# Performance work log

Measured on AMD Instinct MI355X. Metric: run time of the kernel, lower is better.

Reference implementation:

```python
import jax, jax.numpy as jnp
import numpy as np

EPS = 1e-4
GROUPS = 8


def setup_inputs() -> dict:
    key = jax.random.key(0)
    k1, k2 = jax.random.split(key)
    N, C, H, W = 64, 512, 32, 32
    x = jax.random.normal(k1, (N, C, H, W), dtype=jnp.float32)
    weight = jax.random.uniform(k2, (C, 1), dtype=jnp.float32)  # torch reset: uniform_()
    bias = jnp.zeros((C, 1), dtype=jnp.float32)
    return {"x": x, "weight": weight, "bias": bias}


def _whiten_group(cov):
    # cov: [L, L] symmetric PSD. torch.svd on symmetric PSD gives descending
    # eigenvalues e and eigenvectors in v's columns.
    _, e, vh = jnp.linalg.svd(cov)
    v = vh.T
    L = e.shape[0]
    # Faithful reproduction of the source's counter_i logic:
    # counter_i = 1 unless some eigenvalue <= eps, then counter_i = first such j + 1.
    hit = e <= EPS
    counter = jnp.where(jnp.any(hit), jnp.argmax(hit) + 1, 1)
    keep = jnp.arange(L) < counter
    w = jnp.where(keep, jax.lax.rsqrt(e), 0.0)
    # subspace = sum_j v_j * rsqrt(e_j) * v_j^T over kept j
    return (v * w[None, :]) @ v.T


def reference(x, weight, bias):
    N, C, H, W = x.shape
    G = GROUPS
    L = C // G
    M = N * H * W
    xf = jnp.transpose(x, (1, 0, 2, 3)).reshape(C, M)  # [C, N*H*W]
    mu = xf.mean(1, keepdims=True)
    xc = xf - mu
    xg = xc.reshape(G, L, M)
    # Diagonal blocks of (x x^T / M + eps*I): [G, L, L]
    cov = jnp.einsum('glm,gkm->glk', xg, xg) / M + EPS * jnp.eye(L, dtype=xg.dtype)
    sub = jax.vmap(_whiten_group)(cov)  # [G, L, L]
    xr = jnp.einsum('glk,gkm->glm', sub, xg).reshape(C, M)
    xr = xr * weight + bias
    return jnp.transpose(xr.reshape(C, N, H, W), (1, 0, 2, 3))
```

## Files before the change

### kernel.cpp

```cpp
#include <hip/hip_runtime.h>

#define HW    1024
#define C_CH  512


__global__ __launch_bounds__(256, 8) void cov_kernel(const float* __restrict__ x,
                                                     float* __restrict__ Spart,
                                                     float* __restrict__ chansum) {
  const int ks = blockIdx.x & 3;
  const int n  = (blockIdx.x >> 2) & 63;
  const int g  = blockIdx.x >> 8;
  __shared__ __align__(16) float As[4096];
  const int t  = threadIdx.x;
  const int ti = t >> 4;
  const int tj = t & 15;
  float acc[4][4];
#pragma unroll
  for (int r = 0; r < 4; r++)
#pragma unroll
    for (int s = 0; s < 4; s++) acc[r][s] = 0.f;
  float rsum = 0.f;

  const float* base = x + ((size_t)(n * C_CH + g * 64)) * HW;
  const int rlo = t >> 4;
  const int cc  = t & 15;

  for (int chunk = 0; chunk < 4; chunk++) {
    const int k0 = ks * 256 + chunk * 64;
#pragma unroll
    for (int s = 0; s < 4; s++) {
      const int row = 16 * s + rlo;
      const float4 v = *(const float4*)(base + (size_t)row * HW + k0 + 4 * cc);
      const int w0 = 4 * ((row >> 2) ^ cc) + (row & 3);
      As[(4 * cc + 0) * 64 + w0] = v.x;
      As[(4 * cc + 1) * 64 + w0] = v.y;
      As[(4 * cc + 2) * 64 + w0] = v.z;
      As[(4 * cc + 3) * 64 + w0] = v.w;
    }
    __syncthreads();
#pragma unroll 16
    for (int kk = 0; kk < 64; kk++) {
      const int kq = kk >> 2;
      const float4 a = *(const float4*)&As[kk * 64 + 4 * (ti ^ kq)];
      const float4 b = *(const float4*)&As[kk * 64 + 4 * (tj ^ kq)];
      acc[0][0] += a.x * b.x; acc[0][1] += a.x * b.y; acc[0][2] += a.x * b.z; acc[0][3] += a.x * b.w;
      acc[1][0] += a.y * b.x; acc[1][1] += a.y * b.y; acc[1][2] += a.y * b.z; acc[1][3] += a.y * b.w;
      acc[2][0] += a.z * b.x; acc[2][1] += a.z * b.y; acc[2][2] += a.z * b.z; acc[2][3] += a.z * b.w;
      acc[3][0] += a.w * b.x; acc[3][1] += a.w * b.y; acc[3][2] += a.w * b.z; acc[3][3] += a.w * b.w;
    }
    if (t < 64) {
      float s2 = 0.f;
#pragma unroll 16
      for (int kk = 0; kk < 64; kk++)
        s2 += As[kk * 64 + 4 * ((t >> 2) ^ (kk >> 2)) + (t & 3)];
      rsum += s2;
    }
    __syncthreads();
  }

  float* P = Spart + ((size_t)(g * 256 + n * 4 + ks)) * 4096;
#pragma unroll
  for (int r = 0; r < 4; r++) {
    float4 w4;
    w4.x = acc[r][0]; w4.y = acc[r][1]; w4.z = acc[r][2]; w4.w = acc[r][3];
    *(float4*)&P[(4 * ti + r) * 64 + 4 * tj] = w4;
  }
  if (t < 64) atomicAdd(&chansum[g * 64 + t], rsum);
}

__global__ __launch_bounds__(256) void reduce_kernel(const float* __restrict__ Spart,
                                                     float* __restrict__ S) {
  const int q   = blockIdx.x >> 7;
  const int idx = (blockIdx.x & 127) * 256 + threadIdx.x;
  const int g   = idx >> 12;
  const int e   = idx & 4095;
  const float* P = Spart + ((size_t)(g * 256 + q * 64)) * 4096 + e;
  float s = 0.f;
#pragma unroll 8
  for (int p = 0; p < 64; p++) s += P[(size_t)p * 4096];
  atomicAdd(&S[idx], s);
}

__global__ __launch_bounds__(256) void eigen_kernel(
    const float* __restrict__ S, const float* __restrict__ chansum,
    const float* __restrict__ weight, const float* __restrict__ bias,
    float* __restrict__ v0f, float* __restrict__ w2, float* __restrict__ b2) {
  const int g = blockIdx.x;
  __shared__ __align__(16) float Bf[64 * 68];
  __shared__ double Cd[64][65];
  __shared__ double vv[64], uu[64];
  __shared__ double dred;
  __shared__ float f32red;
  __shared__ int ired;
  const int t  = threadIdx.x;
  const int ti = t >> 4, tj = t & 15;
  const double Minv = 1.0 / 65536.0;

  for (int idx = t; idx < 4096; idx += 256) {
    const int i = idx >> 6, j = idx & 63;
    const double mui = (double)chansum[g * 64 + i] * Minv;
    const double muj = (double)chansum[g * 64 + j] * Minv;
    Cd[i][j] = (double)S[g * 4096 + idx] * Minv - mui * muj + (i == j ? 1e-4 : 0.0);
  }
  __syncthreads();
  if (t < 64) {
    double d = Cd[t][t];
#pragma unroll
    for (int off = 32; off; off >>= 1) d = fmin(d, __shfl_down(d, off));
    if (t == 0) f32red = (float)(0.49 * fmax(d, 0.0));
  }
  __syncthreads();
  const float sg = f32red;
  for (int idx = t; idx < 4096; idx += 256) {
    const int i = idx >> 6, j = idx & 63;
    Bf[i * 68 + j] = (float)Cd[i][j] - (i == j ? sg : 0.f);
  }
  __syncthreads();

  for (int it = 0; it < 12; it++) {
    if (t < 64) {
      float tr = Bf[t * 68 + t];
#pragma unroll
      for (int off = 32; off; off >>= 1) tr += __shfl_down(tr, off);
      if (t == 0) f32red = 1.f / tr;
    }
    __syncthreads();
    const float sc = f32red, scl = sc * sc;
    float acc[4][4];
#pragma unroll
    for (int r = 0; r < 4; r++)
#pragma unroll
      for (int s = 0; s < 4; s++) acc[r][s] = 0.f;
#pragma unroll 16
    for (int kk = 0; kk < 64; kk++) {
      const float4 a = *(const float4*)&Bf[kk * 68 + 4 * ti];
      const float4 b = *(const float4*)&Bf[kk * 68 + 4 * tj];
      acc[0][0] += a.x * b.x; acc[0][1] += a.x * b.y; acc[0][2] += a.x * b.z; acc[0][3] += a.x * b.w;
      acc[1][0] += a.y * b.x; acc[1][1] += a.y * b.y; acc[1][2] += a.y * b.z; acc[1][3] += a.y * b.w;
      acc[2][0] += a.z * b.x; acc[2][1] += a.z * b.y; acc[2][2] += a.z * b.z; acc[2][3] += a.z * b.w;
      acc[3][0] += a.w * b.x; acc[3][1] += a.w * b.y; acc[3][2] += a.w * b.z; acc[3][3] += a.w * b.w;
    }
    __syncthreads();
#pragma unroll
    for (int r = 0; r < 4; r++) {
      float4 w4;
      w4.x = acc[r][0] * scl; w4.y = acc[r][1] * scl;
      w4.z = acc[r][2] * scl; w4.w = acc[r][3] * scl;
      *(float4*)&Bf[(4 * ti + r) * 68 + 4 * tj] = w4;
    }
    __syncthreads();
  }

  if (t < 64) {
    float d = Bf[t * 68 + t];
    int bj = t;
#pragma unroll
    for (int off = 32; off; off >>= 1) {
      const float od = __shfl_down(d, off);
      const int   oj = __shfl_down(bj, off);
      if (od > d) { d = od; bj = oj; }
    }
    if (t == 0) ired = bj;
  }
  __syncthreads();
  const int jstar = ired;
  if (t < 64) vv[t] = (double)Bf[t * 68 + jstar];
  __syncthreads();

  for (int pi = 0; pi < 3; pi++) {
    if (t < 64) {
      double s = 0.0;
      for (int k = 0; k < 64; k++) s += Cd[t][k] * vv[k];
      uu[t] = s;
    }
    __syncthreads();
    if (t < 64) {
      double q = uu[t] * uu[t];
#pragma unroll
      for (int off = 32; off; off >>= 1) q += __shfl_down(q, off);
      if (t == 0) dred = 1.0 / sqrt(q);
    }
    __syncthreads();
    if (t < 64) vv[t] = uu[t] * dred;
    __syncthreads();
  }
  if (t < 64) {
    double s = 0.0;
    for (int k = 0; k < 64; k++) s += Cd[t][k] * vv[k];
    uu[t] = s;
  }
  __syncthreads();
  if (t < 64) {
    double q = vv[t] * uu[t];
#pragma unroll
    for (int off = 32; off; off >>= 1) q += __shfl_down(q, off);
    if (t == 0) dred = 1.0 / sqrt(q);
  }
  __syncthreads();
  const double rsl = dred;
  double w2v = 0.0;
  if (t < 64) {
    const int c = g * 64 + t;
    v0f[c] = (float)vv[t];
    w2v = (double)weight[c] * rsl * vv[t];
    w2[c] = (float)w2v;
  }
  __syncthreads();
  if (t < 64) {
    double q = vv[t] * ((double)chansum[g * 64 + t] * Minv);
#pragma unroll
    for (int off = 32; off; off >>= 1) q += __shfl_down(q, off);
    if (t == 0) dred = q;
  }
  __syncthreads();
  if (t < 64) {
    const int c = g * 64 + t;
    b2[c] = (float)((double)bias[c] - w2v * dred);
  }
}

__global__ __launch_bounds__(256, 8) void apply_kernel(
    const float* __restrict__ x, const float* __restrict__ v0f,
    const float* __restrict__ w2, const float* __restrict__ b2,
    float* __restrict__ out) {
  const int q = blockIdx.x & 3;
  const int n = (blockIdx.x >> 2) & 63;
  const int g = blockIdx.x >> 8;
  __shared__ float vs[64], wsh[64], bsh[64];
  const int t = threadIdx.x;
  if (t < 64) {
    vs[t]  = v0f[g * 64 + t];
    wsh[t] = w2[g * 64 + t];
    bsh[t] = b2[g * 64 + t];
  }
  __syncthreads();
  const size_t boff = ((size_t)(n * C_CH + g * 64)) * HW + q * 256 + t;
  const float* base = x + boff;
  float p = 0.f;
#pragma unroll 8
  for (int l = 0; l < 64; l++) p += vs[l] * base[(size_t)l * HW];
  float* ob = out + boff;
#pragma unroll 8
  for (int l = 0; l < 64; l++) ob[(size_t)l * HW] = wsh[l] * p + bsh[l];
}

extern "C" void kernel_launch(void* const* d_in, const int* in_sizes, int n_in,
                              void* d_out, int out_size, void* d_ws, size_t ws_size,
                              hipStream_t stream) {
  const float* x      = (const float*)d_in[0];
  const float* weight = (const float*)d_in[1];
  const float* bias   = (const float*)d_in[2];
  float* out = (float*)d_out;
  float* ws  = (float*)d_ws;

  float* S       = ws;
  float* chansum = ws + 32768;
  float* v0f     = ws + 33280;
  float* w2      = ws + 33792;
  float* b2      = ws + 34304;
  float* Spart   = out;

  hipMemsetAsync(d_ws, 0, (32768 + 512) * sizeof(float), stream);

  cov_kernel<<<dim3(2048), dim3(256), 0, stream>>>(x, Spart, chansum);
  reduce_kernel<<<dim3(512), dim3(256), 0, stream>>>(Spart, S);
  eigen_kernel<<<dim3(8), dim3(256), 0, stream>>>(S, chansum, weight, bias,
                                                  v0f, w2, b2);
  apply_kernel<<<dim3(2048), dim3(256), 0, stream>>>(x, v0f, w2, b2, out);
}
```

Baseline: 324.8 us.

## Exploit Gram symmetry, halve K-splits, drop atomics, vectorize apply kernel

The covariance and eigen power-iteration GEMMs now compute only the upper-triangular 4x4 tiles (136 of 256 threads active) and mirror them into the lower half on store, which halves the FMA work. The cov kernel splits K in two instead of four. This halves the partial-sum buffer, so the reduce kernel sums 128 partials per element with a plain store and no atomics or memset of S. The apply kernel processes a whole image plane per block with float4 loads and stores. The cost is idle threads in the GEMM loops and lower block counts and parallelism in cov, reduce and apply.

```diff
diff --git a/kernel.cpp b/kernel.cpp
--- a/kernel.cpp
+++ b/kernel.cpp
@@ -4,16 +4,21 @@
 #define C_CH  512
 
 
-__global__ __launch_bounds__(256, 8) void cov_kernel(const float* __restrict__ x,
+__global__ __launch_bounds__(256, 4) void cov_kernel(const float* __restrict__ x,
                                                      float* __restrict__ Spart,
                                                      float* __restrict__ chansum) {
-  const int ks = blockIdx.x & 3;
-  const int n  = (blockIdx.x >> 2) & 63;
-  const int g  = blockIdx.x >> 8;
+  const int ks = blockIdx.x & 1;
+  const int n  = (blockIdx.x >> 1) & 63;
+  const int g  = blockIdx.x >> 7;
   __shared__ __align__(16) float As[4096];
-  const int t  = threadIdx.x;
-  const int ti = t >> 4;
-  const int tj = t & 15;
+  const int t = threadIdx.x;
+
+  int ti = 0, rem = t;
+  while (ti < 16 && rem >= 16 - ti) { rem -= 16 - ti; ++ti; }
+  const bool act = (t < 136);
+  const int tj = act ? ti + rem : 0;
+  if (!act) ti = 0;
+
   float acc[4][4];
 #pragma unroll
   for (int r = 0; r < 4; r++)
@@ -25,8 +30,8 @@
   const int rlo = t >> 4;
   const int cc  = t & 15;
 
-  for (int chunk = 0; chunk < 4; chunk++) {
-    const int k0 = ks * 256 + chunk * 64;
+  for (int chunk = 0; chunk < 8; chunk++) {
+    const int k0 = ks * 512 + chunk * 64;
 #pragma unroll
     for (int s = 0; s < 4; s++) {
       const int row = 16 * s + rlo;
@@ -38,15 +43,17 @@
       As[(4 * cc + 3) * 64 + w0] = v.w;
     }
     __syncthreads();
+    if (act) {
 #pragma unroll 16
-    for (int kk = 0; kk < 64; kk++) {
-      const int kq = kk >> 2;
-      const float4 a = *(const float4*)&As[kk * 64 + 4 * (ti ^ kq)];
-      const float4 b = *(const float4*)&As[kk * 64 + 4 * (tj ^ kq)];
-      acc[0][0] += a.x * b.x; acc[0][1] += a.x * b.y; acc[0][2] += a.x * b.z; acc[0][3] += a.x * b.w;
-      acc[1][0] += a.y * b.x; acc[1][1] += a.y * b.y; acc[1][2] += a.y * b.z; acc[1][3] += a.y * b.w;
-      acc[2][0] += a.z * b.x; acc[2][1] += a.z * b.y; acc[2][2] += a.z * b.z; acc[2][3] += a.z * b.w;
-      acc[3][0] += a.w * b.x; acc[3][1] += a.w * b.y; acc[3][2] += a.w * b.z; acc[3][3] += a.w * b.w;
+      for (int kk = 0; kk < 64; kk++) {
+        const int kq = kk >> 2;
+        const float4 a = *(const float4*)&As[kk * 64 + 4 * (ti ^ kq)];
+        const float4 b = *(const float4*)&As[kk * 64 + 4 * (tj ^ kq)];
+        acc[0][0] += a.x * b.x; acc[0][1] += a.x * b.y; acc[0][2] += a.x * b.z; acc[0][3] += a.x * b.w;
+        acc[1][0] += a.y * b.x; acc[1][1] += a.y * b.y; acc[1][2] += a.y * b.z; acc[1][3] += a.y * b.w;
+        acc[2][0] += a.z * b.x; acc[2][1] += a.z * b.y; acc[2][2] += a.z * b.z; acc[2][3] += a.z * b.w;
+        acc[3][0] += a.w * b.x; acc[3][1] += a.w * b.y; acc[3][2] += a.w * b.z; acc[3][3] += a.w * b.w;
+      }
     }
     if (t < 64) {
       float s2 = 0.f;
@@ -58,27 +65,36 @@
     __syncthreads();
   }
 
-  float* P = Spart + ((size_t)(g * 256 + n * 4 + ks)) * 4096;
-#pragma unroll
-  for (int r = 0; r < 4; r++) {
-    float4 w4;
-    w4.x = acc[r][0]; w4.y = acc[r][1]; w4.z = acc[r][2]; w4.w = acc[r][3];
-    *(float4*)&P[(4 * ti + r) * 64 + 4 * tj] = w4;
+  float* P = Spart + ((size_t)(g * 128 + n * 2 + ks)) * 4096;
+  if (act) {
+#pragma unroll
+    for (int r = 0; r < 4; r++) {
+      float4 w4;
+      w4.x = acc[r][0]; w4.y = acc[r][1]; w4.z = acc[r][2]; w4.w = acc[r][3];
+      *(float4*)&P[(4 * ti + r) * 64 + 4 * tj] = w4;
+    }
+    if (ti != tj) {
+#pragma unroll
+      for (int s = 0; s < 4; s++) {
+        float4 w4;
+        w4.x = acc[0][s]; w4.y = acc[1][s]; w4.z = acc[2][s]; w4.w = acc[3][s];
+        *(float4*)&P[(4 * tj + s) * 64 + 4 * ti] = w4;
+      }
+    }
   }
   if (t < 64) atomicAdd(&chansum[g * 64 + t], rsum);
 }
 
 __global__ __launch_bounds__(256) void reduce_kernel(const float* __restrict__ Spart,
                                                      float* __restrict__ S) {
-  const int q   = blockIdx.x >> 7;
-  const int idx = (blockIdx.x & 127) * 256 + threadIdx.x;
+  const int idx = blockIdx.x * 256 + threadIdx.x;
   const int g   = idx >> 12;
   const int e   = idx & 4095;
-  const float* P = Spart + ((size_t)(g * 256 + q * 64)) * 4096 + e;
+  const float* P = Spart + ((size_t)(g * 128)) * 4096 + e;
   float s = 0.f;
-#pragma unroll 8
-  for (int p = 0; p < 64; p++) s += P[(size_t)p * 4096];
-  atomicAdd(&S[idx], s);
+#pragma unroll 16
+  for (int p = 0; p < 128; p++) s += P[(size_t)p * 4096];
+  S[idx] = s;
 }
 
 __global__ __launch_bounds__(256) void eigen_kernel(
@@ -92,9 +108,14 @@
   __shared__ double dred;
   __shared__ float f32red;
   __shared__ int ired;
-  const int t  = threadIdx.x;
-  const int ti = t >> 4, tj = t & 15;
+  const int t = threadIdx.x;
   const double Minv = 1.0 / 65536.0;
+
+  int ti = 0, rem = t;
+  while (ti < 16 && rem >= 16 - ti) { rem -= 16 - ti; ++ti; }
+  const bool act = (t < 136);
+  const int tj = act ? ti + rem : 0;
+  if (!act) ti = 0;
 
   for (int idx = t; idx < 4096; idx += 256) {
     const int i = idx >> 6, j = idx & 63;
@@ -131,22 +152,35 @@
     for (int r = 0; r < 4; r++)
 #pragma unroll
       for (int s = 0; s < 4; s++) acc[r][s] = 0.f;
+    if (act) {
 #pragma unroll 16
-    for (int kk = 0; kk < 64; kk++) {
-      const float4 a = *(const float4*)&Bf[kk * 68 + 4 * ti];
-      const float4 b = *(const float4*)&Bf[kk * 68 + 4 * tj];
-      acc[0][0] += a.x * b.x; acc[0][1] += a.x * b.y; acc[0][2] += a.x * b.z; acc[0][3] += a.x * b.w;
-      acc[1][0] += a.y * b.x; acc[1][1] += a.y * b.y; acc[1][2] += a.y * b.z; acc[1][3] += a.y * b.w;
-      acc[2][0] += a.z * b.x; acc[2][1] += a.z * b.y; acc[2][2] += a.z * b.z; acc[2][3] += a.z * b.w;
-      acc[3][0] += a.w * b.x; acc[3][1] += a.w * b.y; acc[3][2] += a.w * b.z; acc[3][3] += a.w * b.w;
-    }
-    __syncthreads();
-#pragma unroll
-    for (int r = 0; r < 4; r++) {
-      float4 w4;
-      w4.x = acc[r][0] * scl; w4.y = acc[r][1] * scl;
-      w4.z = acc[r][2] * scl; w4.w = acc[r][3] * scl;
-      *(float4*)&Bf[(4 * ti + r) * 68 + 4 * tj] = w4;
+      for (int kk = 0; kk < 64; kk++) {
+        const float4 a = *(const float4*)&Bf[kk * 68 + 4 * ti];
+        const float4 b = *(const float4*)&Bf[kk * 68 + 4 * tj];
+        acc[0][0] += a.x * b.x; acc[0][1] += a.x * b.y; acc[0][2] += a.x * b.z; acc[0][3] += a.x * b.w;
+        acc[1][0] += a.y * b.x; acc[1][1] += a.y * b.y; acc[1][2] += a.y * b.z; acc[1][3] += a.y * b.w;
+        acc[2][0] += a.z * b.x; acc[2][1] += a.z * b.y; acc[2][2] += a.z * b.z; acc[2][3] += a.z * b.w;
+        acc[3][0] += a.w * b.x; acc[3][1] += a.w * b.y; acc[3][2] += a.w * b.z; acc[3][3] += a.w * b.w;
+      }
+    }
+    __syncthreads();
+    if (act) {
+#pragma unroll
+      for (int r = 0; r < 4; r++) {
+        float4 w4;
+        w4.x = acc[r][0] * scl; w4.y = acc[r][1] * scl;
+        w4.z = acc[r][2] * scl; w4.w = acc[r][3] * scl;
+        *(float4*)&Bf[(4 * ti + r) * 68 + 4 * tj] = w4;
+      }
+      if (ti != tj) {
+#pragma unroll
+        for (int s = 0; s < 4; s++) {
+          float4 w4;
+          w4.x = acc[0][s] * scl; w4.y = acc[1][s] * scl;
+          w4.z = acc[2][s] * scl; w4.w = acc[3][s] * scl;
+          *(float4*)&Bf[(4 * tj + s) * 68 + 4 * ti] = w4;
+        }
+      }
     }
     __syncthreads();
   }
@@ -219,13 +253,12 @@
   }
 }
 
-__global__ __launch_bounds__(256, 8) void apply_kernel(
+__global__ __launch_bounds__(256) void apply_kernel(
     const float* __restrict__ x, const float* __restrict__ v0f,
     const float* __restrict__ w2, const float* __restrict__ b2,
     float* __restrict__ out) {
-  const int q = blockIdx.x & 3;
-  const int n = (blockIdx.x >> 2) & 63;
-  const int g = blockIdx.x >> 8;
+  const int n = blockIdx.x & 63;
+  const int g = blockIdx.x >> 6;
   __shared__ float vs[64], wsh[64], bsh[64];
   const int t = threadIdx.x;
   if (t < 64) {
@@ -234,14 +267,23 @@
     bsh[t] = b2[g * 64 + t];
   }
   __syncthreads();
-  const size_t boff = ((size_t)(n * C_CH + g * 64)) * HW + q * 256 + t;
-  const float* base = x + boff;
-  float p = 0.f;
+  const size_t boff = ((size_t)(n * C_CH + g * 64)) * HW + 4 * t;
+  const float4* bx = (const float4*)(x + boff);
+  float4 p = make_float4(0.f, 0.f, 0.f, 0.f);
 #pragma unroll 8
-  for (int l = 0; l < 64; l++) p += vs[l] * base[(size_t)l * HW];
-  float* ob = out + boff;
+  for (int l = 0; l < 64; l++) {
+    const float4 v = bx[(size_t)l * (HW / 4)];
+    p.x += vs[l] * v.x; p.y += vs[l] * v.y;
+    p.z += vs[l] * v.z; p.w += vs[l] * v.w;
+  }
+  float4* bo = (float4*)(out + boff);
 #pragma unroll 8
-  for (int l = 0; l < 64; l++) ob[(size_t)l * HW] = wsh[l] * p + bsh[l];
+  for (int l = 0; l < 64; l++) {
+    float4 o;
+    o.x = wsh[l] * p.x + bsh[l]; o.y = wsh[l] * p.y + bsh[l];
+    o.z = wsh[l] * p.z + bsh[l]; o.w = wsh[l] * p.w + bsh[l];
+    bo[(size_t)l * (HW / 4)] = o;
+  }
 }
 
 extern "C" void kernel_launch(void* const* d_in, const int* in_sizes, int n_in,
@@ -260,11 +302,11 @@
   float* b2      = ws + 34304;
   float* Spart   = out;
 
-  hipMemsetAsync(d_ws, 0, (32768 + 512) * sizeof(float), stream);
-
-  cov_kernel<<<dim3(2048), dim3(256), 0, stream>>>(x, Spart, chansum);
-  reduce_kernel<<<dim3(512), dim3(256), 0, stream>>>(Spart, S);
+  hipMemsetAsync((char*)d_ws + 32768 * sizeof(float), 0, 512 * sizeof(float), stream);
+
+  cov_kernel<<<dim3(1024), dim3(256), 0, stream>>>(x, Spart, chansum);
+  reduce_kernel<<<dim3(128), dim3(256), 0, stream>>>(Spart, S);
   eigen_kernel<<<dim3(8), dim3(256), 0, stream>>>(S, chansum, weight, bias,
                                                   v0f, w2, b2);
-  apply_kernel<<<dim3(2048), dim3(256), 0, stream>>>(x, v0f, w2, b2, out);
-}
+  apply_kernel<<<dim3(512), dim3(256), 0, stream>>>(x, v0f, w2, b2, out);
+}
```

Result: slower. 340.9 us (+4.9%).

## Compute group covariance with split-bf16 MFMA and one block per sample-group

Applied to the files above, without the earlier changes.

Replaces the scalar FP32 Gram-matrix loop in the covariance kernel with bf16 MFMA 32x32x16 instructions. Each value is split into high and low bf16 parts and four MFMAs per tile recover close to FP32 accuracy. Each block now covers one full (sample, group) slice with double-buffered register prefetch, and the four waves' partial sums are combined in LDS. This cuts the partial count from 256 to 64 per group, so the reduce kernel writes directly without atomics and the memset shrinks. The cost is reduced occupancy and a small loss of precision relative to true FP32.

```diff
diff --git a/kernel.cpp b/kernel.cpp
--- a/kernel.cpp
+++ b/kernel.cpp
@@ -3,82 +3,157 @@
 #define HW    1024
 #define C_CH  512
 
-
-__global__ __launch_bounds__(256, 8) void cov_kernel(const float* __restrict__ x,
+typedef __attribute__((ext_vector_type(8)))  short bfrag;
+typedef __attribute__((ext_vector_type(16))) float f32x16;
+
+
+__global__ __launch_bounds__(256, 2) void cov_kernel(const float* __restrict__ x,
                                                      float* __restrict__ Spart,
                                                      float* __restrict__ chansum) {
-  const int ks = blockIdx.x & 3;
-  const int n  = (blockIdx.x >> 2) & 63;
-  const int g  = blockIdx.x >> 8;
-  __shared__ __align__(16) float As[4096];
-  const int t  = threadIdx.x;
-  const int ti = t >> 4;
-  const int tj = t & 15;
-  float acc[4][4];
-#pragma unroll
-  for (int r = 0; r < 4; r++)
-#pragma unroll
-    for (int s = 0; s < 4; s++) acc[r][s] = 0.f;
-  float rsum = 0.f;
-
-  const float* base = x + ((size_t)(n * C_CH + g * 64)) * HW;
-  const int rlo = t >> 4;
-  const int cc  = t & 15;
-
-  for (int chunk = 0; chunk < 4; chunk++) {
-    const int k0 = ks * 256 + chunk * 64;
-#pragma unroll
-    for (int s = 0; s < 4; s++) {
-      const int row = 16 * s + rlo;
-      const float4 v = *(const float4*)(base + (size_t)row * HW + k0 + 4 * cc);
-      const int w0 = 4 * ((row >> 2) ^ cc) + (row & 3);
-      As[(4 * cc + 0) * 64 + w0] = v.x;
-      As[(4 * cc + 1) * 64 + w0] = v.y;
-      As[(4 * cc + 2) * 64 + w0] = v.z;
-      As[(4 * cc + 3) * 64 + w0] = v.w;
-    }
-    __syncthreads();
-#pragma unroll 16
-    for (int kk = 0; kk < 64; kk++) {
-      const int kq = kk >> 2;
-      const float4 a = *(const float4*)&As[kk * 64 + 4 * (ti ^ kq)];
-      const float4 b = *(const float4*)&As[kk * 64 + 4 * (tj ^ kq)];
-      acc[0][0] += a.x * b.x; acc[0][1] += a.x * b.y; acc[0][2] += a.x * b.z; acc[0][3] += a.x * b.w;
-      acc[1][0] += a.y * b.x; acc[1][1] += a.y * b.y; acc[1][2] += a.y * b.z; acc[1][3] += a.y * b.w;
-      acc[2][0] += a.z * b.x; acc[2][1] += a.z * b.y; acc[2][2] += a.z * b.z; acc[2][3] += a.z * b.w;
-      acc[3][0] += a.w * b.x; acc[3][1] += a.w * b.y; acc[3][2] += a.w * b.z; acc[3][3] += a.w * b.w;
-    }
-    if (t < 64) {
-      float s2 = 0.f;
-#pragma unroll 16
-      for (int kk = 0; kk < 64; kk++)
-        s2 += As[kk * 64 + 4 * ((t >> 2) ^ (kk >> 2)) + (t & 3)];
-      rsum += s2;
-    }
-    __syncthreads();
-  }
-
-  float* P = Spart + ((size_t)(g * 256 + n * 4 + ks)) * 4096;
-#pragma unroll
-  for (int r = 0; r < 4; r++) {
-    float4 w4;
-    w4.x = acc[r][0]; w4.y = acc[r][1]; w4.z = acc[r][2]; w4.w = acc[r][3];
-    *(float4*)&P[(4 * ti + r) * 64 + 4 * tj] = w4;
-  }
-  if (t < 64) atomicAdd(&chansum[g * 64 + t], rsum);
+  const int n = blockIdx.x & 63;
+  const int g = blockIdx.x >> 6;
+  __shared__ __align__(16) unsigned short LDSbuf[2 * 64 * 128];
+  unsigned short* Ahi = LDSbuf;
+  unsigned short* Alo = LDSbuf + 64 * 128;
+
+  const int t   = threadIdx.x;
+  const int row = t >> 2;
+  const int kq  = t & 3;
+  const int l   = t & 63;
+  const int w   = t >> 6;
+
+  const float* rowp = x + ((size_t)(n * C_CH + g * 64) + row) * HW + kq * 32;
+
+  f32x16 acc00 = {}, acc01 = {}, acc10 = {}, acc11 = {};
+  float psum = 0.f;
+  float4 buf0[8], buf1[8];
+
+  auto LOADC = [&](float4* buf, int c) {
+#pragma unroll
+    for (int i = 0; i < 8; i++)
+      buf[i] = *(const float4*)(rowp + c * 128 + 4 * i);
+  };
+
+  auto CVTW = [&](const float4* buf) {
+#pragma unroll
+    for (int p = 0; p < 4; p++) {
+      const float xs[8] = {buf[2 * p].x, buf[2 * p].y, buf[2 * p].z, buf[2 * p].w,
+                           buf[2 * p + 1].x, buf[2 * p + 1].y, buf[2 * p + 1].z, buf[2 * p + 1].w};
+      unsigned int hu[8], lw[8];
+#pragma unroll
+      for (int e = 0; e < 8; e++) {
+        const float xv = xs[e];
+        const unsigned int u  = __float_as_uint(xv);
+        const unsigned int r  = u + 0x7FFFu + ((u >> 16) & 1u);
+        const unsigned int hb = r & 0xFFFF0000u;
+        const float lof = xv - __uint_as_float(hb);
+        const unsigned int v  = __float_as_uint(lof);
+        const unsigned int lr = v + 0x7FFFu + ((v >> 16) & 1u);
+        hu[e] = hb >> 16;
+        lw[e] = lr >> 16;
+        psum += xv;
+      }
+      uint4 hp, lp;
+      hp.x = hu[0] | (hu[1] << 16); hp.y = hu[2] | (hu[3] << 16);
+      hp.z = hu[4] | (hu[5] << 16); hp.w = hu[6] | (hu[7] << 16);
+      lp.x = lw[0] | (lw[1] << 16); lp.y = lw[2] | (lw[3] << 16);
+      lp.z = lw[4] | (lw[5] << 16); lp.w = lw[6] | (lw[7] << 16);
+      const int slot = (kq * 4 + p) ^ (row & 7);
+      *(uint4*)&Ahi[row * 128 + slot * 8] = hp;
+      *(uint4*)&Alo[row * 128 + slot * 8] = lp;
+    }
+  };
+
+  auto COMPUTE = [&]() {
+#pragma unroll
+    for (int k4 = 0; k4 < 2; k4++) {
+      const int kl = w * 2 + k4;
+      const int sp = kl * 2 + (l >> 5);
+      const int r0 = l & 31;
+      const int ph = sp ^ (r0 & 7);
+      const int i0 = r0 * 128 + ph * 8;
+      const int i1 = (32 + r0) * 128 + ph * 8;
+      const bfrag hA0 = *(const bfrag*)&Ahi[i0];
+      const bfrag hA1 = *(const bfrag*)&Ahi[i1];
+      const bfrag lA0 = *(const bfrag*)&Alo[i0];
+      const bfrag lA1 = *(const bfrag*)&Alo[i1];
+      acc00 = __builtin_amdgcn_mfma_f32_32x32x16_bf16(hA0, hA0, acc00, 0, 0, 0);
+      acc00 = __builtin_amdgcn_mfma_f32_32x32x16_bf16(hA0, lA0, acc00, 0, 0, 0);
+      acc00 = __builtin_amdgcn_mfma_f32_32x32x16_bf16(lA0, hA0, acc00, 0, 0, 0);
+      acc00 = __builtin_amdgcn_mfma_f32_32x32x16_bf16(lA0, lA0, acc00, 0, 0, 0);
+      acc01 = __builtin_amdgcn_mfma_f32_32x32x16_bf16(hA0, hA1, acc01, 0, 0, 0);
+      acc01 = __builtin_amdgcn_mfma_f32_32x32x16_bf16(hA0, lA1, acc01, 0, 0, 0);
+      acc01 = __builtin_amdgcn_mfma_f32_32x32x16_bf16(lA0, hA1, acc01, 0, 0, 0);
+      acc01 = __builtin_amdgcn_mfma_f32_32x32x16_bf16(lA0, lA1, acc01, 0, 0, 0);
+      acc10 = __builtin_amdgcn_mfma_f32_32x32x16_bf16(hA1, hA0, acc10, 0, 0, 0);
+      acc10 = __builtin_amdgcn_mfma_f32_32x32x16_bf16(hA1, lA0, acc10, 0, 0, 0);
+      acc10 = __builtin_amdgcn_mfma_f32_32x32x16_bf16(lA1, hA0, acc10, 0, 0, 0);
+      acc10 = __builtin_amdgcn_mfma_f32_32x32x16_bf16(lA1, lA0, acc10, 0, 0, 0);
+      acc11 = __builtin_amdgcn_mfma_f32_32x32x16_bf16(hA1, hA1, acc11, 0, 0, 0);
+      acc11 = __builtin_amdgcn_mfma_f32_32x32x16_bf16(hA1, lA1, acc11, 0, 0, 0);
+      acc11 = __builtin_amdgcn_mfma_f32_32x32x16_bf16(lA1, hA1, acc11, 0, 0, 0);
+      acc11 = __builtin_amdgcn_mfma_f32_32x32x16_bf16(lA1, lA1, acc11, 0, 0, 0);
+    }
+  };
+
+  LOADC(buf0, 0); CVTW(buf0); __syncthreads();
+  LOADC(buf1, 1); COMPUTE(); __syncthreads(); CVTW(buf1); __syncthreads();
+  LOADC(buf0, 2); COMPUTE(); __syncthreads(); CVTW(buf0); __syncthreads();
+  LOADC(buf1, 3); COMPUTE(); __syncthreads(); CVTW(buf1); __syncthreads();
+  LOADC(buf0, 4); COMPUTE(); __syncthreads(); CVTW(buf0); __syncthreads();
+  LOADC(buf1, 5); COMPUTE(); __syncthreads(); CVTW(buf1); __syncthreads();
+  LOADC(buf0, 6); COMPUTE(); __syncthreads(); CVTW(buf0); __syncthreads();
+  LOADC(buf1, 7); COMPUTE(); __syncthreads(); CVTW(buf1); __syncthreads();
+  COMPUTE();
+  __syncthreads();
+
+  float* R0 = (float*)LDSbuf;
+  float* R1 = R0 + 4096;
+  const int coff  = l & 31;
+  const int rbase = 4 * (l >> 5);
+  float* Rw = (w & 1) ? R1 : R0;
+  if (w < 2) {
+#pragma unroll
+    for (int e = 0; e < 16; e++) {
+      const int ri = (e & 3) + 8 * (e >> 2) + rbase;
+      Rw[ri * 64 + coff]             = acc00[e];
+      Rw[ri * 64 + 32 + coff]        = acc01[e];
+      Rw[(32 + ri) * 64 + coff]      = acc10[e];
+      Rw[(32 + ri) * 64 + 32 + coff] = acc11[e];
+    }
+  }
+  __syncthreads();
+  if (w >= 2) {
+#pragma unroll
+    for (int e = 0; e < 16; e++) {
+      const int ri = (e & 3) + 8 * (e >> 2) + rbase;
+      Rw[ri * 64 + coff]             += acc00[e];
+      Rw[ri * 64 + 32 + coff]        += acc01[e];
+      Rw[(32 + ri) * 64 + coff]      += acc10[e];
+      Rw[(32 + ri) * 64 + 32 + coff] += acc11[e];
+    }
+  }
+  __syncthreads();
+  float* P = Spart + (size_t)blockIdx.x * 4096;
+  for (int idx = t; idx < 4096; idx += 256)
+    P[idx] = R0[idx] + R1[idx];
+
+  float s = psum;
+  s += __shfl_down(s, 2);
+  s += __shfl_down(s, 1);
+  if ((t & 3) == 0) atomicAdd(&chansum[g * 64 + row], s);
 }
 
 __global__ __launch_bounds__(256) void reduce_kernel(const float* __restrict__ Spart,
                                                      float* __restrict__ S) {
-  const int q   = blockIdx.x >> 7;
-  const int idx = (blockIdx.x & 127) * 256 + threadIdx.x;
+  const int idx = blockIdx.x * 256 + threadIdx.x;
   const int g   = idx >> 12;
   const int e   = idx & 4095;
-  const float* P = Spart + ((size_t)(g * 256 + q * 64)) * 4096 + e;
+  const float* P = Spart + ((size_t)(g * 64)) * 4096 + e;
   float s = 0.f;
 #pragma unroll 8
   for (int p = 0; p < 64; p++) s += P[(size_t)p * 4096];
-  atomicAdd(&S[idx], s);
+  S[idx] = s;
 }
 
 __global__ __launch_bounds__(256) void eigen_kernel(
@@ -260,10 +335,10 @@
   float* b2      = ws + 34304;
   float* Spart   = out;
 
-  hipMemsetAsync(d_ws, 0, (32768 + 512) * sizeof(float), stream);
-
-  cov_kernel<<<dim3(2048), dim3(256), 0, stream>>>(x, Spart, chansum);
-  reduce_kernel<<<dim3(512), dim3(256), 0, stream>>>(Spart, S);
+  hipMemsetAsync((char*)d_ws + 32768 * sizeof(float), 0, 512 * sizeof(float), stream);
+
+  cov_kernel<<<dim3(512), dim3(256), 0, stream>>>(x, Spart, chansum);
+  reduce_kernel<<<dim3(128), dim3(256), 0, stream>>>(Spart, S);
   eigen_kernel<<<dim3(8), dim3(256), 0, stream>>>(S, chansum, weight, bias,
                                                   v0f, w2, b2);
   apply_kernel<<<dim3(2048), dim3(256), 0, stream>>>(x, v0f, w2, b2, out);
```

Result: slower. 414.3 us (+27.5%).
